# Kernel tuning notes

Measured on AMD Instinct MI355X. Metric: run time of the kernel, lower is better.

Reference implementation:

```python
import jax, jax.numpy as jnp
import numpy as np

N_NODES = 5000
N_EDGES = 50000
HIDDEN = 64
EDGE_DIM = 16


def setup_inputs() -> dict:
    key = jax.random.key(0)
    ks = jax.random.split(key, 8)
    d = HIDDEN
    h = jax.random.normal(ks[0], (N_NODES, d), dtype=jnp.float32)
    edge_index = jax.random.randint(ks[1], (2, N_EDGES), 0, N_NODES, dtype=jnp.int64)
    edge_features = jax.random.normal(ks[2], (N_EDGES, EDGE_DIM), dtype=jnp.float32)
    # edge-network MLP: Linear(edge_dim, d) -> ReLU -> Linear(d, d*d)
    W1 = jax.random.normal(ks[3], (EDGE_DIM, d), dtype=jnp.float32) * (1.0 / np.sqrt(EDGE_DIM))
    b1 = jnp.zeros((d,), dtype=jnp.float32)
    W2 = jax.random.normal(ks[4], (d, d * d), dtype=jnp.float32) * (1.0 / np.sqrt(d))
    b2 = jnp.zeros((d * d,), dtype=jnp.float32)
    # GRUCell params (torch layout: rows = [reset; update; new])
    W_ih = jax.random.normal(ks[5], (3 * d, d), dtype=jnp.float32) * (1.0 / np.sqrt(d))
    W_hh = jax.random.normal(ks[6], (3 * d, d), dtype=jnp.float32) * (1.0 / np.sqrt(d))
    b_ih = jnp.zeros((3 * d,), dtype=jnp.float32)
    b_hh = jnp.zeros((3 * d,), dtype=jnp.float32)
    return {"h": h, "edge_index": edge_index, "edge_features": edge_features,
            "W1": W1, "b1": b1, "W2": W2, "b2": b2,
            "W_ih": W_ih, "W_hh": W_hh, "b_ih": b_ih, "b_hh": b_hh}


def reference(h, edge_index, edge_features, W1, b1, W2, b2, W_ih, W_hh, b_ih, b_hh):
    n_nodes, d = h.shape
    src, tgt = edge_index[0], edge_index[1]
    # 1) gather sender states
    h_w = h[src]  # (E, d)
    # 2-3) edge MLP -> per-edge transformation matrices (E, d, d)
    A = jax.nn.relu(edge_features @ W1 + b1) @ W2 + b2
    A = A.reshape(-1, d, d)
    # 4) per-edge matvec messages
    msg = jnp.einsum('eij,ej->ei', A, h_w)  # (E, d)
    # 5) scatter-sum aggregation per target node
    m = jax.ops.segment_sum(msg, tgt, num_segments=n_nodes)  # (N, d)
    # 6) GRUCell(m, h) - torch semantics
    gi = m @ W_ih.T + b_ih   # (N, 3d)
    gh = h @ W_hh.T + b_hh   # (N, 3d)
    i_r, i_z, i_n = jnp.split(gi, 3, axis=-1)
    h_r, h_z, h_n = jnp.split(gh, 3, axis=-1)
    r = jax.nn.sigmoid(i_r + h_r)
    z = jax.nn.sigmoid(i_z + h_z)
    n = jnp.tanh(i_n + r * h_n)
    h_new = (1.0 - z) * n + z * h
    return h_new
```

## Files before the change

kernel.cpp:

```cpp
#include <hip/hip_runtime.h>
#include <math.h>

#define N_NODES 5000
#define N_EDGES 50000
#define POISON_I ((int)0xAAAAAAAAu)

typedef _Float16 f16x8 __attribute__((ext_vector_type(8)));
typedef _Float16 f16x4 __attribute__((ext_vector_type(4)));
typedef _Float16 f16x2 __attribute__((ext_vector_type(2)));
typedef float    f32x4 __attribute__((ext_vector_type(4)));

static __device__ __forceinline__ f32x4 mfma16f(f16x8 a, f16x8 b, f32x4 c) {
    return __builtin_amdgcn_mfma_f32_16x16x32_f16(a, b, c, 0, 0, 0);
}
static __device__ __forceinline__ f32x4 mfma16k16(f16x4 a, f16x4 b, f32x4 c) {
    return __builtin_amdgcn_mfma_f32_16x16x16f16(a, b, c, 0, 0, 0);
}

__global__ void prep_kernel(const float* __restrict__ W2, const float* __restrict__ b2,
                            const float* __restrict__ Wih, const float* __restrict__ Whh,
                            const int* __restrict__ ei,
                            _Float16* __restrict__ Br, _Float16* __restrict__ Bg2,
                            int* __restrict__ cnt,
                            _Float16* __restrict__ T, _Float16* __restrict__ Hh,
                            _Float16* __restrict__ Hl) {
    int g = blockIdx.x * 256 + threadIdx.x;
    if (g < 33792) {
        int nt = g / 8448, rem = g - nt * 8448;
        int ks = rem >> 6, lane = rem & 63;
        int lo = lane & 15, q = lane >> 4;
        int i = nt * 16 + lo, kap0 = ks * 32 + q * 8;
        f16x8 v;
#pragma unroll
        for (int p = 0; p < 8; ++p) {
            int kap = kap0 + p;
            int k2 = kap >> 7, rem2 = kap & 127;
            int j = rem2 >> 1, k = k2 * 2 + (rem2 & 1);
            float x = 0.f;
            if (k < 64) x = W2[(size_t)k * 4096 + i * 64 + j];
            else if (k == 64) x = b2[i * 64 + j];
            v[p] = (_Float16)x;
        }
        *(f16x8*)(Br + (size_t)g * 8) = v;
        return;
    }
    g -= 33792;
    if (g < 3072) {
        int ct = g >> 7, ks = (g >> 6) & 1, lane = g & 63;
        int lo = lane & 15, q = lane >> 4;
        const float* src = (ct < 12) ? Wih : Whh;
        int r = ((ct < 12) ? ct : ct - 12) * 16 + lo;
        int j0 = ks * 32 + q * 8;
        f16x8 v;
#pragma unroll
        for (int p = 0; p < 8; ++p) v[p] = (_Float16)src[r * 64 + j0 + p];
        *(f16x8*)(Bg2 + (size_t)g * 8) = v;
        return;
    }
    g -= 3072;
    if (g < N_EDGES) {
        atomicAdd(&cnt[ei[N_EDGES + g]], 1);
        return;
    }
    g -= N_EDGES;
    if (g < 64) {
        T [(size_t)N_EDGES * 64 + g] = (_Float16)0.f;
        Hh[(size_t)N_EDGES * 64 + g] = (_Float16)0.f;
        Hl[(size_t)N_EDGES * 64 + g] = (_Float16)0.f;
    }
}

__global__ __launch_bounds__(1024) void scan_kernel(const int* __restrict__ cnt,
                                                    int* __restrict__ off,
                                                    int* __restrict__ cur) {
    __shared__ int s[1024];
    int tid = threadIdx.x;
    int base = tid * 5;
    int loc[5]; int sum = 0;
#pragma unroll
    for (int q = 0; q < 5; ++q) {
        int v = (base + q < N_NODES) ? (cnt[base + q] - POISON_I) : 0;
        loc[q] = sum; sum += v;
    }
    s[tid] = sum; __syncthreads();
    for (int d = 1; d < 1024; d <<= 1) {
        int v = (tid >= d) ? s[tid - d] : 0;
        __syncthreads();
        s[tid] += v;
        __syncthreads();
    }
    int excl = (tid > 0) ? s[tid - 1] : 0;
#pragma unroll
    for (int q = 0; q < 5; ++q)
        if (base + q < N_NODES) { off[base + q] = excl + loc[q]; cur[base + q] = excl + loc[q]; }
    if (tid == 1023) off[N_NODES] = excl + sum;
}

__global__ __launch_bounds__(256) void edge_stage(
    const int* __restrict__ ei, const float* __restrict__ ef,
    const float* __restrict__ W1, const float* __restrict__ b1,
    const float* __restrict__ h, int* __restrict__ cur,
    _Float16* __restrict__ T, _Float16* __restrict__ Hh,
    _Float16* __restrict__ Hl) {
    int w = threadIdx.x >> 6, lane = threadIdx.x & 63;
    int e = blockIdx.x * 4 + w;
    int src = ei[e], tgt = ei[N_EDGES + e];
    int q;
    if (lane == 0) q = atomicAdd(&cur[tgt], 1);
    q = __shfl(q, 0);
    float hv = h[(size_t)src * 64 + lane];
    _Float16 hh = (_Float16)hv;
    _Float16 hl = (_Float16)(hv - (float)hh);
    const float* efr = ef + (size_t)e * 16;
    float tacc = b1[lane];
#pragma unroll
    for (int k = 0; k < 16; ++k) tacc += efr[k] * W1[k * 64 + lane];
    T [(size_t)q * 64 + lane] = (_Float16)fmaxf(tacc, 0.f);
    Hh[(size_t)q * 64 + lane] = hh;
    Hl[(size_t)q * 64 + lane] = hl;
}

__global__ __launch_bounds__(1024) void node_gnn(
    const int* __restrict__ toff, const _Float16* __restrict__ T,
    const _Float16* __restrict__ Hh, const _Float16* __restrict__ Hl,
    const _Float16* __restrict__ Br, const _Float16* __restrict__ Bg2,
    const float* __restrict__ h, const float* __restrict__ bih,
    const float* __restrict__ bhh, float* __restrict__ out)
{
    extern __shared__ __align__(16) char smem[];
    _Float16* As   = (_Float16*)smem;
    float*    mbuf  = (float*)smem;
    _Float16* mls   = (_Float16*)(smem + 12480);
    _Float16* hls16 = (_Float16*)(smem + 14784);
    float*    gbuf  = (float*)(smem + 33024);
    float*    Svec  = (float*)(smem + 57664);
    int*      nsl   = (int*)(smem + 61760);

    int tid = threadIdx.x, w16 = tid >> 6, lane = tid & 63;
    int lo = lane & 15, q = lane >> 4;
    int nt = w16 & 3, kq = w16 >> 2;
    int m0 = blockIdx.x * 16;

    if (tid < 17) {
        int nn = m0 + tid; if (nn > N_NODES) nn = N_NODES;
        nsl[tid] = toff[nn];
    }
    __syncthreads();
    int base = nsl[w16], deg = nsl[w16 + 1] - base;

    f32x4 z4 = {0.f, 0.f, 0.f, 0.f};
    f32x4 acc[4][4];
#pragma unroll
    for (int a = 0; a < 4; ++a)
#pragma unroll
        for (int b = 0; b < 4; ++b) acc[a][b] = z4;
    float sp[4] = {0.f, 0.f, 0.f, 0.f};

    int nw = (deg + 15) >> 4;
    for (int ws = 0; ws < nw; ++ws) {
        int ri[4];
#pragma unroll
        for (int k = 0; k < 4; ++k) {
            int s = ws * 16 + q * 4 + k;
            ri[k] = (s < deg) ? (base + s) : N_EDGES;
        }
        f16x4 at[4], bh[4], bl[4];
#pragma unroll
        for (int mi = 0; mi < 4; ++mi)
#pragma unroll
            for (int k = 0; k < 4; ++k)
                at[mi][k] = T[(size_t)ri[k] * 64 + mi * 16 + lo];
#pragma unroll
        for (int ni = 0; ni < 4; ++ni)
#pragma unroll
            for (int k = 0; k < 4; ++k) {
                bh[ni][k] = Hh[(size_t)ri[k] * 64 + ni * 16 + lo];
                bl[ni][k] = Hl[(size_t)ri[k] * 64 + ni * 16 + lo];
            }
#pragma unroll
        for (int ni = 0; ni < 4; ++ni)
#pragma unroll
            for (int mi = 0; mi < 4; ++mi) {
                acc[mi][ni] = mfma16k16(at[mi], bh[ni], acc[mi][ni]);
                acc[mi][ni] = mfma16k16(at[mi], bl[ni], acc[mi][ni]);
            }
#pragma unroll
        for (int ni = 0; ni < 4; ++ni) {
            float s4 = 0.f;
#pragma unroll
            for (int k = 0; k < 4; ++k)
                s4 += (float)bh[ni][k] + (float)bl[ni][k];
            sp[ni] += s4;
        }
    }
#pragma unroll
    for (int ni = 0; ni < 4; ++ni) {
        float v = sp[ni];
        v += __shfl_xor(v, 16);
        v += __shfl_xor(v, 32);
        if (q == 0) Svec[w16 * 64 + ni * 16 + lo] = v;
    }

    const f16x8* BrV = (const f16x8*)Br;
    f32x4 macc = {0.f, 0.f, 0.f, 0.f};
#pragma unroll
    for (int kc = 0; kc < 4; ++kc) {
        _Float16* aw = As + w16 * 1032;
#pragma unroll
        for (int ni = 0; ni < 4; ++ni)
#pragma unroll
            for (int g0 = 0; g0 < 4; g0 += 2) {
                int k2l = q * 2 + (g0 >> 1);
                f16x2 pv = { (_Float16)acc[kc][ni][g0], (_Float16)acc[kc][ni][g0 + 1] };
                *(f16x2*)(aw + k2l * 128 + (ni * 16 + lo) * 2) = pv;
            }
        __syncthreads();
        const _Float16* Arow = As + lo * 1032 + q * 8;
#pragma unroll
        for (int s = 0; s < 8; ++s) {
            int ksl = kq * 8 + s;
            f16x8 a = *(const f16x8*)(Arow + ksl * 32);
            f16x8 bfr = BrV[(size_t)(nt * 132 + kc * 32 + ksl) * 64 + lane];
            macc = mfma16f(a, bfr, macc);
        }
        __syncthreads();
    }
    {
        float sacc = Svec[w16 * 64 + lane];
        f16x2 pv = { (_Float16)sacc, (_Float16)0.f };
        *(f16x2*)(As + w16 * 1032 + lane * 2) = pv;
    }
    __syncthreads();
    {
        f16x8 a = *(const f16x8*)(As + lo * 1032 + kq * 32 + q * 8);
        f16x8 bfr = BrV[(size_t)(nt * 132 + 128 + kq) * 64 + lane];
        macc = mfma16f(a, bfr, macc);
    }
    __syncthreads();
    if (kq > 0) {
#pragma unroll
        for (int g = 0; g < 4; ++g)
            mbuf[(kq - 1) * 1040 + (q * 4 + g) * 65 + nt * 16 + lo] = macc[g];
    }
    if (kq == 3) {
        int t2 = nt * 64 + lane;
#pragma unroll
        for (int r = 0; r < 4; ++r) {
            int e2 = r * 256 + t2, nl = e2 >> 6, j = e2 & 63;
            int n = m0 + nl;
            float hv = (n < N_NODES) ? h[(size_t)n * 64 + j] : 0.f;
            hls16[nl * 72 + j] = (_Float16)hv;
        }
    }
    __syncthreads();
    if (kq == 0) {
#pragma unroll
        for (int g = 0; g < 4; ++g) {
            float mv = macc[g];
#pragma unroll
            for (int pp = 0; pp < 3; ++pp)
                mv += mbuf[pp * 1040 + (q * 4 + g) * 65 + nt * 16 + lo];
            mls[(q * 4 + g) * 72 + nt * 16 + lo] = (_Float16)mv;
        }
    }
    __syncthreads();
    if (w16 < 8) {
        int w8 = w16;
        f16x8 am0 = *(const f16x8*)&mls[lo * 72 + q * 8];
        f16x8 am1 = *(const f16x8*)&mls[lo * 72 + 32 + q * 8];
        f16x8 ah0 = *(const f16x8*)&hls16[lo * 72 + q * 8];
        f16x8 ah1 = *(const f16x8*)&hls16[lo * 72 + 32 + q * 8];
        const f16x8* BgV = (const f16x8*)Bg2;
        f32x4 ga[3] = {z4, z4, z4};
#pragma unroll
        for (int j = 0; j < 3; ++j) {
            int ct = w8 + 8 * j;
            f16x8 bg0 = BgV[(size_t)(ct * 2 + 0) * 64 + lane];
            f16x8 bg1 = BgV[(size_t)(ct * 2 + 1) * 64 + lane];
            f16x8 a0f = (ct < 12) ? am0 : ah0;
            f16x8 a1f = (ct < 12) ? am1 : ah1;
            ga[j] = mfma16f(a0f, bg0, ga[j]);
            ga[j] = mfma16f(a1f, bg1, ga[j]);
        }
#pragma unroll
        for (int j = 0; j < 3; ++j) {
            int ct = w8 + 8 * j;
            int col = (ct < 12) ? (ct * 16 + lo) : (192 + (ct - 12) * 16 + lo);
#pragma unroll
            for (int g = 0; g < 4; ++g) gbuf[(q * 4 + g) * 385 + col] = ga[j][g];
        }
    }
    __syncthreads();
    if (w16 < 8) {
        int i = lane;
#pragma unroll
        for (int u = 0; u < 2; ++u) {
            int nl = w16 * 2 + u, n = m0 + nl;
            if (n >= N_NODES) continue;
            const float* gb = gbuf + nl * 385;
            float ir  = gb[i]       + bih[i];
            float iz  = gb[64 + i]  + bih[64 + i];
            float inn = gb[128 + i] + bih[128 + i];
            float hr  = gb[192 + i] + bhh[i];
            float hz  = gb[256 + i] + bhh[64 + i];
            float hn  = gb[320 + i] + bhh[128 + i];
            float hval = h[(size_t)n * 64 + i];
            float r = 1.f / (1.f + expf(-(ir + hr)));
            float z = 1.f / (1.f + expf(-(iz + hz)));
            float nn = tanhf(inn + r * hn);
            out[n * 64 + i] = (1.f - z) * nn + z * hval;
        }
    }
}

extern "C" void kernel_launch(void* const* d_in, const int* in_sizes, int n_in,
                              void* d_out, int out_size, void* d_ws, size_t ws_size,
                              hipStream_t stream) {
    const float* h   = (const float*)d_in[0];
    const int*   ei  = (const int*)d_in[1];
    const float* ef  = (const float*)d_in[2];
    const float* W1  = (const float*)d_in[3];
    const float* b1  = (const float*)d_in[4];
    const float* W2  = (const float*)d_in[5];
    const float* b2  = (const float*)d_in[6];
    const float* Wih = (const float*)d_in[7];
    const float* Whh = (const float*)d_in[8];
    const float* bih = (const float*)d_in[9];
    const float* bhh = (const float*)d_in[10];
    float* out = (float*)d_out;

    _Float16* T    = (_Float16*)d_ws;
    _Float16* Hh   = T + (size_t)(N_EDGES + 1) * 64;
    _Float16* Hl   = Hh + (size_t)(N_EDGES + 1) * 64;
    _Float16* Br   = Hl + (size_t)(N_EDGES + 1) * 64;
    _Float16* Bg2  = Br + 270336;
    int*      cnt  = (int*)(Bg2 + 24576);
    int*      toff = cnt + N_NODES;
    int*      cur  = toff + N_NODES + 1;

    static bool lds_cfg = false;
    if (!lds_cfg) {
        hipFuncSetAttribute((const void*)node_gnn,
                            hipFuncAttributeMaxDynamicSharedMemorySize, 61952);
        lds_cfg = true;
    }

    prep_kernel<<<340, 256, 0, stream>>>(W2, b2, Wih, Whh, ei, Br, Bg2, cnt,
                                         T, Hh, Hl);
    scan_kernel<<<1, 1024, 0, stream>>>(cnt, toff, cur);
    edge_stage<<<12500, 256, 0, stream>>>(ei, ef, W1, b1, h, cur, T, Hh, Hl);
    node_gnn<<<313, 1024, 61952, stream>>>(toff, T, Hh, Hl, Br, Bg2, h,
                                           bih, bhh, out);
}
```

Baseline: 136.4 us.

## Replace counting-sort CSR build with atomic linked lists and fuse prep kernels

Edges are no longer bucketed by target through count, scan and scatter. Each edge is pushed onto a per-node linked list with atomicExch, and the edge packing and weight packing run in a single launch. The node kernel walks each list serially, gathering up to 16 edge indices per window into shared memory. This removes two kernel launches and the scan. In exchange it adds dependent pointer-chasing loads and non-contiguous row accesses in the aggregation kernel, and it relies on head[] being pre-poisoned.

```diff
diff --git a/kernel.cpp b/kernel.cpp
--- a/kernel.cpp
+++ b/kernel.cpp
@@ -17,14 +17,38 @@
     return __builtin_amdgcn_mfma_f32_16x16x16f16(a, b, c, 0, 0, 0);
 }
 
-__global__ void prep_kernel(const float* __restrict__ W2, const float* __restrict__ b2,
-                            const float* __restrict__ Wih, const float* __restrict__ Whh,
-                            const int* __restrict__ ei,
-                            _Float16* __restrict__ Br, _Float16* __restrict__ Bg2,
-                            int* __restrict__ cnt,
-                            _Float16* __restrict__ T, _Float16* __restrict__ Hh,
-                            _Float16* __restrict__ Hl) {
-    int g = blockIdx.x * 256 + threadIdx.x;
+__global__ __launch_bounds__(256) void edge_pack(
+    const int* __restrict__ ei, const float* __restrict__ ef,
+    const float* __restrict__ W1, const float* __restrict__ b1,
+    const float* __restrict__ h,
+    const float* __restrict__ W2, const float* __restrict__ b2,
+    const float* __restrict__ Wih, const float* __restrict__ Whh,
+    _Float16* __restrict__ T, _Float16* __restrict__ Hh,
+    _Float16* __restrict__ Hl, _Float16* __restrict__ Br,
+    _Float16* __restrict__ Bg2, int* __restrict__ head,
+    int* __restrict__ next) {
+    int blk = blockIdx.x;
+    if (blk < 12500) {
+        int w = threadIdx.x >> 6, lane = threadIdx.x & 63;
+        int e = blk * 4 + w;
+        int src = ei[e], tgt = ei[N_EDGES + e];
+        if (lane == 0) {
+            int old = atomicExch(&head[tgt], e);
+            next[e] = old;
+        }
+        float hv = h[(size_t)src * 64 + lane];
+        _Float16 hh = (_Float16)hv;
+        _Float16 hl = (_Float16)(hv - (float)hh);
+        const float* efr = ef + (size_t)e * 16;
+        float tacc = b1[lane];
+#pragma unroll
+        for (int k = 0; k < 16; ++k) tacc += efr[k] * W1[k * 64 + lane];
+        T [(size_t)e * 64 + lane] = (_Float16)fmaxf(tacc, 0.f);
+        Hh[(size_t)e * 64 + lane] = hh;
+        Hl[(size_t)e * 64 + lane] = hl;
+        return;
+    }
+    int g = (blk - 12500) * 256 + threadIdx.x;
     if (g < 33792) {
         int nt = g / 8448, rem = g - nt * 8448;
         int ks = rem >> 6, lane = rem & 63;
@@ -47,10 +71,10 @@
     g -= 33792;
     if (g < 3072) {
         int ct = g >> 7, ks = (g >> 6) & 1, lane = g & 63;
-        int lo = lane & 15, q = lane >> 4;
+        int lo = lane & 15;
         const float* src = (ct < 12) ? Wih : Whh;
         int r = ((ct < 12) ? ct : ct - 12) * 16 + lo;
-        int j0 = ks * 32 + q * 8;
+        int j0 = ks * 32 + (lane >> 4) * 8;
         f16x8 v;
 #pragma unroll
         for (int p = 0; p < 8; ++p) v[p] = (_Float16)src[r * 64 + j0 + p];
@@ -58,11 +82,6 @@
         return;
     }
     g -= 3072;
-    if (g < N_EDGES) {
-        atomicAdd(&cnt[ei[N_EDGES + g]], 1);
-        return;
-    }
-    g -= N_EDGES;
     if (g < 64) {
         T [(size_t)N_EDGES * 64 + g] = (_Float16)0.f;
         Hh[(size_t)N_EDGES * 64 + g] = (_Float16)0.f;
@@ -70,62 +89,13 @@
     }
 }
 
-__global__ __launch_bounds__(1024) void scan_kernel(const int* __restrict__ cnt,
-                                                    int* __restrict__ off,
-                                                    int* __restrict__ cur) {
-    __shared__ int s[1024];
-    int tid = threadIdx.x;
-    int base = tid * 5;
-    int loc[5]; int sum = 0;
-#pragma unroll
-    for (int q = 0; q < 5; ++q) {
-        int v = (base + q < N_NODES) ? (cnt[base + q] - POISON_I) : 0;
-        loc[q] = sum; sum += v;
-    }
-    s[tid] = sum; __syncthreads();
-    for (int d = 1; d < 1024; d <<= 1) {
-        int v = (tid >= d) ? s[tid - d] : 0;
-        __syncthreads();
-        s[tid] += v;
-        __syncthreads();
-    }
-    int excl = (tid > 0) ? s[tid - 1] : 0;
-#pragma unroll
-    for (int q = 0; q < 5; ++q)
-        if (base + q < N_NODES) { off[base + q] = excl + loc[q]; cur[base + q] = excl + loc[q]; }
-    if (tid == 1023) off[N_NODES] = excl + sum;
-}
-
-__global__ __launch_bounds__(256) void edge_stage(
-    const int* __restrict__ ei, const float* __restrict__ ef,
-    const float* __restrict__ W1, const float* __restrict__ b1,
-    const float* __restrict__ h, int* __restrict__ cur,
-    _Float16* __restrict__ T, _Float16* __restrict__ Hh,
-    _Float16* __restrict__ Hl) {
-    int w = threadIdx.x >> 6, lane = threadIdx.x & 63;
-    int e = blockIdx.x * 4 + w;
-    int src = ei[e], tgt = ei[N_EDGES + e];
-    int q;
-    if (lane == 0) q = atomicAdd(&cur[tgt], 1);
-    q = __shfl(q, 0);
-    float hv = h[(size_t)src * 64 + lane];
-    _Float16 hh = (_Float16)hv;
-    _Float16 hl = (_Float16)(hv - (float)hh);
-    const float* efr = ef + (size_t)e * 16;
-    float tacc = b1[lane];
-#pragma unroll
-    for (int k = 0; k < 16; ++k) tacc += efr[k] * W1[k * 64 + lane];
-    T [(size_t)q * 64 + lane] = (_Float16)fmaxf(tacc, 0.f);
-    Hh[(size_t)q * 64 + lane] = hh;
-    Hl[(size_t)q * 64 + lane] = hl;
-}
-
 __global__ __launch_bounds__(1024) void node_gnn(
-    const int* __restrict__ toff, const _Float16* __restrict__ T,
-    const _Float16* __restrict__ Hh, const _Float16* __restrict__ Hl,
-    const _Float16* __restrict__ Br, const _Float16* __restrict__ Bg2,
-    const float* __restrict__ h, const float* __restrict__ bih,
-    const float* __restrict__ bhh, float* __restrict__ out)
+    const int* __restrict__ head, const int* __restrict__ next,
+    const _Float16* __restrict__ T, const _Float16* __restrict__ Hh,
+    const _Float16* __restrict__ Hl, const _Float16* __restrict__ Br,
+    const _Float16* __restrict__ Bg2, const float* __restrict__ h,
+    const float* __restrict__ bih, const float* __restrict__ bhh,
+    float* __restrict__ out)
 {
     extern __shared__ __align__(16) char smem[];
     _Float16* As   = (_Float16*)smem;
@@ -134,19 +104,13 @@
     _Float16* hls16 = (_Float16*)(smem + 14784);
     float*    gbuf  = (float*)(smem + 33024);
     float*    Svec  = (float*)(smem + 57664);
-    int*      nsl   = (int*)(smem + 61760);
+    int*      widx  = (int*)(smem + 61760);
 
     int tid = threadIdx.x, w16 = tid >> 6, lane = tid & 63;
     int lo = lane & 15, q = lane >> 4;
     int nt = w16 & 3, kq = w16 >> 2;
     int m0 = blockIdx.x * 16;
-
-    if (tid < 17) {
-        int nn = m0 + tid; if (nn > N_NODES) nn = N_NODES;
-        nsl[tid] = toff[nn];
-    }
-    __syncthreads();
-    int base = nsl[w16], deg = nsl[w16 + 1] - base;
+    int n = m0 + w16;
 
     f32x4 z4 = {0.f, 0.f, 0.f, 0.f};
     f32x4 acc[4][4];
@@ -156,13 +120,20 @@
         for (int b = 0; b < 4; ++b) acc[a][b] = z4;
     float sp[4] = {0.f, 0.f, 0.f, 0.f};
 
-    int nw = (deg + 15) >> 4;
-    for (int ws = 0; ws < nw; ++ws) {
+    int cur = (n < N_NODES) ? head[n] : POISON_I;
+    cur = __builtin_amdgcn_readfirstlane(cur);
+    while (cur != POISON_I) {
+        int wcnt = 0;
+        do {
+            widx[w16 * 16 + wcnt] = cur;
+            ++wcnt;
+            cur = __builtin_amdgcn_readfirstlane(next[cur]);
+        } while (cur != POISON_I && wcnt < 16);
         int ri[4];
 #pragma unroll
         for (int k = 0; k < 4; ++k) {
-            int s = ws * 16 + q * 4 + k;
-            ri[k] = (s < deg) ? (base + s) : N_EDGES;
+            int s = q * 4 + k;
+            ri[k] = (s < wcnt) ? widx[w16 * 16 + s] : N_EDGES;
         }
         f16x4 at[4], bh[4], bl[4];
 #pragma unroll
@@ -247,8 +218,8 @@
 #pragma unroll
         for (int r = 0; r < 4; ++r) {
             int e2 = r * 256 + t2, nl = e2 >> 6, j = e2 & 63;
-            int n = m0 + nl;
-            float hv = (n < N_NODES) ? h[(size_t)n * 64 + j] : 0.f;
+            int nn = m0 + nl;
+            float hv = (nn < N_NODES) ? h[(size_t)nn * 64 + j] : 0.f;
             hls16[nl * 72 + j] = (_Float16)hv;
         }
     }
@@ -295,8 +266,8 @@
         int i = lane;
 #pragma unroll
         for (int u = 0; u < 2; ++u) {
-            int nl = w16 * 2 + u, n = m0 + nl;
-            if (n >= N_NODES) continue;
+            int nl = w16 * 2 + u, nn = m0 + nl;
+            if (nn >= N_NODES) continue;
             const float* gb = gbuf + nl * 385;
             float ir  = gb[i]       + bih[i];
             float iz  = gb[64 + i]  + bih[64 + i];
@@ -304,11 +275,11 @@
             float hr  = gb[192 + i] + bhh[i];
             float hz  = gb[256 + i] + bhh[64 + i];
             float hn  = gb[320 + i] + bhh[128 + i];
-            float hval = h[(size_t)n * 64 + i];
+            float hval = h[(size_t)nn * 64 + i];
             float r = 1.f / (1.f + expf(-(ir + hr)));
             float z = 1.f / (1.f + expf(-(iz + hz)));
-            float nn = tanhf(inn + r * hn);
-            out[n * 64 + i] = (1.f - z) * nn + z * hval;
+            float nnv = tanhf(inn + r * hn);
+            out[nn * 64 + i] = (1.f - z) * nnv + z * hval;
         }
     }
 }
@@ -334,21 +305,18 @@
     _Float16* Hl   = Hh + (size_t)(N_EDGES + 1) * 64;
     _Float16* Br   = Hl + (size_t)(N_EDGES + 1) * 64;
     _Float16* Bg2  = Br + 270336;
-    int*      cnt  = (int*)(Bg2 + 24576);
-    int*      toff = cnt + N_NODES;
-    int*      cur  = toff + N_NODES + 1;
+    int*      head = (int*)(Bg2 + 24576);
+    int*      next = head + N_NODES;
 
     static bool lds_cfg = false;
     if (!lds_cfg) {
         hipFuncSetAttribute((const void*)node_gnn,
-                            hipFuncAttributeMaxDynamicSharedMemorySize, 61952);
+                            hipFuncAttributeMaxDynamicSharedMemorySize, 62976);
         lds_cfg = true;
     }
 
-    prep_kernel<<<340, 256, 0, stream>>>(W2, b2, Wih, Whh, ei, Br, Bg2, cnt,
-                                         T, Hh, Hl);
-    scan_kernel<<<1, 1024, 0, stream>>>(cnt, toff, cur);
-    edge_stage<<<12500, 256, 0, stream>>>(ei, ef, W1, b1, h, cur, T, Hh, Hl);
-    node_gnn<<<313, 1024, 61952, stream>>>(toff, T, Hh, Hl, Br, Bg2, h,
+    edge_pack<<<12645, 256, 0, stream>>>(ei, ef, W1, b1, h, W2, b2, Wih, Whh,
+                                         T, Hh, Hl, Br, Bg2, head, next);
+    node_gnn<<<313, 1024, 62976, stream>>>(head, next, T, Hh, Hl, Br, Bg2, h,
                                            bih, bhh, out);
 }
```

After: 132.5 us. -2.9%, faster.
